# Performance work log

Hardware: AMD Instinct MI355X
Metric: run time of the kernel (lower is better)

Reference implementation:

```python
import jax, jax.numpy as jnp
import numpy as np

NUM_HEADS = 16
HEAD_SIZE = 64
LN_EPS = 1e-5


def setup_inputs() -> dict:
    key = jax.random.key(0)
    k1, k2, k3 = jax.random.split(key, 3)
    b, l, hidden = 2, 2048, 1024
    qkv_out = HEAD_SIZE * NUM_HEADS + 2 * HEAD_SIZE  # 1152
    x = jax.random.normal(k1, (b, l, hidden), dtype=jnp.float32)
    Wqkv = jax.random.normal(k2, (qkv_out, hidden), dtype=jnp.float32) * 0.02
    gamma = jnp.ones((qkv_out,), dtype=jnp.float32)
    beta = jnp.zeros((qkv_out,), dtype=jnp.float32)
    Wfc = jax.random.normal(k3, (hidden, HEAD_SIZE * NUM_HEADS), dtype=jnp.float32) * 0.02
    return {"x": x, "Wqkv": Wqkv, "gamma": gamma, "beta": beta, "Wfc": Wfc}


def reference(x, Wqkv, gamma, beta, Wfc):
    h, d = NUM_HEADS, HEAD_SIZE
    b, l, _ = x.shape
    # fused QKV projection (no bias), then LayerNorm over the FULL qkv dim
    qkv = jnp.einsum('blc,oc->blo', x, Wqkv)  # (b, l, (h+2)*d)
    mu = jnp.mean(qkv, axis=-1, keepdims=True)
    var = jnp.var(qkv, axis=-1, keepdims=True)
    qkv = (qkv - mu) * jax.lax.rsqrt(var + LN_EPS) * gamma + beta
    qkv = qkv.reshape(b, l, h + 2, d)
    k = qkv[:, :, 0, :]       # (b, l, d) shared K head
    v = qkv[:, :, 1, :]       # (b, l, d) shared V head
    q = qkv[:, :, 2:, :]      # (b, l, h, d) query heads
    scale = 1.0 / np.sqrt(d).astype(np.float32)
    scores = jnp.einsum('bqhd,bkd->bhqk', q, k) * scale  # (b, h, l, l)
    causal = jnp.tril(jnp.ones((l, l), dtype=bool))
    scores = jnp.where(causal, scores, jnp.finfo(scores.dtype).min)
    attn = jax.nn.softmax(scores, axis=-1)
    out = jnp.einsum('bhqk,bkd->bqhd', attn, v).reshape(b, l, h * d)
    return jnp.einsum('blo,ho->blh', out, Wfc)
```

## Files before the change

### kernel.cpp

```cpp
#include <hip/hip_runtime.h>
#include <stdint.h>

typedef __attribute__((ext_vector_type(8))) short s16x8;
typedef __attribute__((ext_vector_type(4))) float f32x4;

#define MFMA16(a, b, c) __builtin_amdgcn_mfma_f32_16x16x32_bf16((a), (b), (c), 0, 0, 0)

__device__ __forceinline__ unsigned short f2bf(float f) {
    unsigned int u = __float_as_uint(f);
    return (unsigned short)((u + 0x7FFFu + ((u >> 16) & 1u)) >> 16);
}
__device__ __forceinline__ float bf2f(unsigned short h) {
    return __uint_as_float(((unsigned int)h) << 16);
}
__device__ __forceinline__ void cvt8(unsigned short* dst, const float* src) {
    const float4 f0 = *(const float4*)(src);
    const float4 f1 = *(const float4*)(src + 4);
    s16x8 v;
    v[0] = (short)f2bf(f0.x); v[1] = (short)f2bf(f0.y);
    v[2] = (short)f2bf(f0.z); v[3] = (short)f2bf(f0.w);
    v[4] = (short)f2bf(f1.x); v[5] = (short)f2bf(f1.y);
    v[6] = (short)f2bf(f1.z); v[7] = (short)f2bf(f1.w);
    *(s16x8*)dst = v;
}
__device__ __forceinline__ void gl_lds16(const unsigned short* g, unsigned short* l) {
    __builtin_amdgcn_global_load_lds(
        (const __attribute__((address_space(1))) unsigned int*)g,
        (__attribute__((address_space(3))) unsigned int*)l,
        16, 0, 0);
}

__global__ __launch_bounds__(256) void cvt_all(const float* __restrict__ x,
                                               const float* __restrict__ wq,
                                               const float* __restrict__ wf,
                                               unsigned short* __restrict__ xb,
                                               unsigned short* __restrict__ wqb,
                                               unsigned short* __restrict__ wfb) {
    const int blk = blockIdx.x;
    const float* src;
    unsigned short* dst;
    int base;
    if (blk < 2048)      { src = x;  dst = xb;  base = blk; }
    else if (blk < 2624) { src = wq; dst = wqb; base = blk - 2048; }
    else                 { src = wf; dst = wfb; base = blk - 2624; }
    const int i = (base * 256 + threadIdx.x) * 8;
    cvt8(&dst[i], &src[i]);
}

template <bool OUT_F32>
__global__ __launch_bounds__(512) void gemm_mn(const unsigned short* __restrict__ A,
                                               const unsigned short* __restrict__ Bw,
                                               void* __restrict__ Cout, int K, int N) {
    const int bm = blockIdx.x, bn = blockIdx.y;
    const int t = threadIdx.x;
    const int lane = t & 63, w = t >> 6;
    const int quad = lane >> 4, col = lane & 15;
    const int wm = (w >> 1) * 32, wn = (w & 1) * 32;

    __shared__ alignas(16) unsigned short As[2][128 * 64];
    __shared__ alignas(16) unsigned short Bs[2][64 * 64];

    f32x4 acc[2][2];
#pragma unroll
    for (int i = 0; i < 2; ++i)
#pragma unroll
        for (int j = 0; j < 2; ++j) acc[i][j] = (f32x4){0.f, 0.f, 0.f, 0.f};

    const int lrow = lane >> 3;
    const int lcol = ((lane & 7) ^ lrow) * 8;
    const unsigned short* Ap = A + (size_t)(bm * 128 + w * 16 + lrow) * K + lcol;
    const unsigned short* Bp = Bw + (size_t)(bn * 64 + w * 8 + lrow) * K + lcol;

#pragma unroll
    for (int j = 0; j < 2; ++j)
        gl_lds16(Ap + (size_t)(j * 8) * K, &As[0][(w * 16 + j * 8) * 64]);
    gl_lds16(Bp, &Bs[0][(w * 8) * 64]);
    __syncthreads();

    const int c7 = col & 7;
    const int fs0 = ((0 * 4 + quad) ^ c7) * 8;
    const int fs1 = ((1 * 4 + quad) ^ c7) * 8;

    for (int k0 = 0; k0 < K; k0 += 64) {
        const int p = (k0 >> 6) & 1;
        if (k0 + 64 < K) {
#pragma unroll
            for (int j = 0; j < 2; ++j)
                gl_lds16(Ap + (size_t)(j * 8) * K + k0 + 64, &As[p ^ 1][(w * 16 + j * 8) * 64]);
            gl_lds16(Bp + k0 + 64, &Bs[p ^ 1][(w * 8) * 64]);
        }
#pragma unroll
        for (int s = 0; s < 2; ++s) {
            const int fs = s ? fs1 : fs0;
            s16x8 af[2], bfr[2];
#pragma unroll
            for (int i = 0; i < 2; ++i)
                af[i] = *(const s16x8*)&As[p][(wm + i * 16 + col) * 64 + fs];
#pragma unroll
            for (int j = 0; j < 2; ++j)
                bfr[j] = *(const s16x8*)&Bs[p][(wn + j * 16 + col) * 64 + fs];
#pragma unroll
            for (int i = 0; i < 2; ++i)
#pragma unroll
                for (int j = 0; j < 2; ++j)
                    acc[i][j] = MFMA16(af[i], bfr[j], acc[i][j]);
        }
        __syncthreads();
    }
    const int rowb = bm * 128 + wm + quad * 4;
    const int colb = bn * 64 + wn + col;
#pragma unroll
    for (int i = 0; i < 2; ++i)
#pragma unroll
        for (int j = 0; j < 2; ++j)
#pragma unroll
            for (int r = 0; r < 4; ++r) {
                size_t off = (size_t)(rowb + i * 16 + r) * N + colb + j * 16;
                if (OUT_F32) ((float*)Cout)[off] = acc[i][j][r];
                else ((unsigned short*)Cout)[off] = f2bf(acc[i][j][r]);
            }
}

__global__ __launch_bounds__(64) void ln_row(unsigned short* __restrict__ qkvn,
                                             const float* __restrict__ gamma,
                                             const float* __restrict__ beta,
                                             unsigned short* __restrict__ vT) {
    const int row = blockIdx.x;
    const int b = row >> 11, l = row & 2047;
    unsigned short* rp = qkvn + (size_t)row * 1152;
    const int lane = threadIdx.x;

    s16x8 v0 = *(const s16x8*)&rp[lane * 8];
    s16x8 v1 = *(const s16x8*)&rp[512 + lane * 8];
    unsigned int v2u = *(const unsigned int*)&rp[1024 + lane * 2];

    float f0[8], f1[8], f2[2];
    float s = 0.f, s2 = 0.f;
#pragma unroll
    for (int e = 0; e < 8; ++e) {
        f0[e] = bf2f((unsigned short)v0[e]);
        f1[e] = bf2f((unsigned short)v1[e]);
        s += f0[e] + f1[e];
        s2 += f0[e] * f0[e] + f1[e] * f1[e];
    }
    f2[0] = bf2f((unsigned short)(v2u & 0xFFFF));
    f2[1] = bf2f((unsigned short)(v2u >> 16));
    s += f2[0] + f2[1];
    s2 += f2[0] * f2[0] + f2[1] * f2[1];

#pragma unroll
    for (int off = 1; off < 64; off <<= 1) {
        s += __shfl_xor(s, off);
        s2 += __shfl_xor(s2, off);
    }
    const float mu = s * (1.0f / 1152.0f);
    float var = s2 * (1.0f / 1152.0f) - mu * mu;
    var = fmaxf(var, 0.0f);
    const float rstd = rsqrtf(var + 1e-5f);

    {
        s16x8 o;
#pragma unroll
        for (int e = 0; e < 8; ++e)
            o[e] = (short)f2bf((f0[e] - mu) * rstd * gamma[lane * 8 + e] + beta[lane * 8 + e]);
        *(s16x8*)&rp[lane * 8] = o;
        if (lane >= 8 && lane < 16) {
            const int d0 = lane * 8 - 64;
#pragma unroll
            for (int e = 0; e < 8; ++e)
                vT[((size_t)(b * 64 + d0 + e)) * 2048 + l] = (unsigned short)o[e];
        }
    }
    {
        s16x8 o;
#pragma unroll
        for (int e = 0; e < 8; ++e)
            o[e] = (short)f2bf((f1[e] - mu) * rstd * gamma[512 + lane * 8 + e] + beta[512 + lane * 8 + e]);
        *(s16x8*)&rp[512 + lane * 8] = o;
    }
    {
        unsigned short o0 = f2bf((f2[0] - mu) * rstd * gamma[1024 + lane * 2] + beta[1024 + lane * 2]);
        unsigned short o1 = f2bf((f2[1] - mu) * rstd * gamma[1025 + lane * 2] + beta[1025 + lane * 2]);
        *(unsigned int*)&rp[1024 + lane * 2] = ((unsigned int)o1 << 16) | o0;
    }
}

__global__ __launch_bounds__(512) void attn_kernel(const unsigned short* __restrict__ qkvn,
                                                   const unsigned short* __restrict__ vT,
                                                   unsigned short* __restrict__ obuf) {
    const int b = blockIdx.x >> 3, hp = blockIdx.x & 7;
    const int yy = blockIdx.y;
    const int qb = (yy < 16) ? (31 - yy) : (yy - 16);
    const int t = threadIdx.x;
    const int lane = t & 63, w = t >> 6;
    const int quad = lane >> 4, col = lane & 15;
    const int hl = w >> 2, wq = w & 3;

    __shared__ alignas(16) unsigned short Ks[2][4096];
    __shared__ alignas(16) unsigned short Vts[2][4096];
    __shared__ alignas(16) unsigned short PQ[8][16][72];

    unsigned short(*Qs)[72] = (unsigned short(*)[72])PQ;

    const int srow = t >> 3;
    const int schunk = t & 7;
    const int ldsoff = srow * 64 + (schunk ^ (srow & 7)) * 8;

#pragma unroll
    for (int hh = 0; hh < 2; ++hh) {
        const unsigned short* qsrc =
            qkvn + (size_t)(b * 2048 + qb * 64 + srow) * 1152 + 128 + (hp * 2 + hh) * 64 + schunk * 8;
        s16x8 v = *(const s16x8*)qsrc;
#pragma unroll
        for (int e = 0; e < 8; ++e)
            v[e] = (short)f2bf(bf2f((unsigned short)v[e]) * 0.125f);
        *(s16x8*)&Qs[hh * 64 + srow][schunk * 8] = v;
    }
    __syncthreads();
    const s16x8 qf0 = *(const s16x8*)&Qs[hl * 64 + wq * 16 + col][quad * 8];
    const s16x8 qf1 = *(const s16x8*)&Qs[hl * 64 + wq * 16 + col][32 + quad * 8];

    const unsigned short* kbase = qkvn + (size_t)(b * 2048 + srow) * 1152 + schunk * 8;
    const unsigned short* vbase = vT + (size_t)(b * 64 + srow) * 2048 + schunk * 8;
    *(uint4*)&Ks[0][ldsoff]  = *(const uint4*)(kbase);
    *(uint4*)&Vts[0][ldsoff] = *(const uint4*)(vbase);
    __syncthreads();

    const int fo0 = col * 128 + ((quad ^ (col & 7)) * 16);
    const int fo1 = col * 128 + (((4 + quad) ^ (col & 7)) * 16);

    s16x8 ones;
#pragma unroll
    for (int e = 0; e < 8; ++e) ones[e] = (short)0x3F80;

    f32x4 Oacc[4];
    f32x4 lacc = {0.f, 0.f, 0.f, 0.f};
#pragma unroll
    for (int nt = 0; nt < 4; ++nt) Oacc[nt] = (f32x4){0.f, 0.f, 0.f, 0.f};

    const int qglob = qb * 64 + wq * 16 + col;
    const int kloc0 = quad * 4;

    for (int kb = 0; kb <= qb; ++kb) {
        const int p = kb & 1;
        uint4 kreg, vreg;
        if (kb < qb) {
            kreg = *(const uint4*)(kbase + (size_t)(kb + 1) * 64 * 1152);
            vreg = *(const uint4*)(vbase + (kb + 1) * 64);
        }
        const bool diag = (kb == qb);
        const char* kb8 = (const char*)Ks[p];
        const char* vb8 = (const char*)Vts[p];

#pragma unroll
        for (int nt = 0; nt < 4; ++nt) {
            s16x8 kf0 = *(const s16x8*)(kb8 + nt * 2048 + fo0);
            s16x8 kf1 = *(const s16x8*)(kb8 + nt * 2048 + fo1);
            f32x4 z = (f32x4){0.f, 0.f, 0.f, 0.f};
            z = MFMA16(kf0, qf0, z);
            z = MFMA16(kf1, qf1, z);
            ushort4 pk;
            unsigned short* pp = (unsigned short*)&pk;
#pragma unroll
            for (int r = 0; r < 4; ++r) {
                float sv = z[r];
                if (diag && (kb * 64 + nt * 16 + kloc0 + r > qglob)) sv = -1e30f;
                pp[r] = f2bf(__expf(sv - 12.0f));
            }
            *(ushort4*)&PQ[w][col][nt * 16 + kloc0] = pk;
        }

        const s16x8 pf0 = *(const s16x8*)&PQ[w][col][quad * 8];
        const s16x8 pf1 = *(const s16x8*)&PQ[w][col][32 + quad * 8];
        lacc = MFMA16(ones, pf0, lacc);
        lacc = MFMA16(ones, pf1, lacc);
#pragma unroll
        for (int nt = 0; nt < 4; ++nt) {
            s16x8 vf0 = *(const s16x8*)(vb8 + nt * 2048 + fo0);
            s16x8 vf1 = *(const s16x8*)(vb8 + nt * 2048 + fo1);
            Oacc[nt] = MFMA16(vf0, pf0, Oacc[nt]);
            Oacc[nt] = MFMA16(vf1, pf1, Oacc[nt]);
        }

        if (kb < qb) {
            *(uint4*)&Ks[p ^ 1][ldsoff]  = kreg;
            *(uint4*)&Vts[p ^ 1][ldsoff] = vreg;
        }
        __syncthreads();
    }

    const int h = hp * 2 + hl;
    const float inv = 1.0f / lacc[0];
    const size_t base = (((size_t)b * 2048 + qglob) * 16 + h) * 64 + kloc0;
#pragma unroll
    for (int nt = 0; nt < 4; ++nt) {
        ushort4 ov;
        unsigned short* op = (unsigned short*)&ov;
#pragma unroll
        for (int r = 0; r < 4; ++r) op[r] = f2bf(Oacc[nt][r] * inv);
        *(ushort4*)&obuf[base + nt * 16] = ov;
    }
}

extern "C" void kernel_launch(void* const* d_in, const int* in_sizes, int n_in,
                              void* d_out, int out_size, void* d_ws, size_t ws_size,
                              hipStream_t stream) {
    (void)in_sizes; (void)n_in; (void)out_size; (void)ws_size;
    const float* x     = (const float*)d_in[0];
    const float* Wqkv  = (const float*)d_in[1];
    const float* gamma = (const float*)d_in[2];
    const float* beta  = (const float*)d_in[3];
    const float* Wfc   = (const float*)d_in[4];
    float* out = (float*)d_out;

    char* ws = (char*)d_ws;
    unsigned short* xb   = (unsigned short*)ws;
    unsigned short* Wqb  = (unsigned short*)(ws + 8388608);
    unsigned short* Wfb  = (unsigned short*)(ws + 10747904);
    unsigned short* qkvn = (unsigned short*)(ws + 12845056);
    unsigned short* vT   = (unsigned short*)(ws + 22282240);
    unsigned short* abuf = (unsigned short*)ws;

    cvt_all<<<dim3(3136), 256, 0, stream>>>(x, Wqkv, Wfc, xb, Wqb, Wfb);
    gemm_mn<false><<<dim3(32, 18), 512, 0, stream>>>(xb, Wqb, qkvn, 1024, 1152);
    ln_row<<<dim3(4096), 64, 0, stream>>>(qkvn, gamma, beta, vT);
    attn_kernel<<<dim3(16, 32), 512, 0, stream>>>(qkvn, vT, abuf);
    gemm_mn<true><<<dim3(32, 16), 512, 0, stream>>>(abuf, Wfb, out, 1024, 1024);
}
```

Baseline: 151.0 us.

## Split attention key tiles across wave pairs and reuse K/V fragments across two query tiles

Each wave now handles 32 queries and half of each 64-key block instead of 16 queries and the full block. Every K and V fragment read from LDS now feeds two query sub-tiles, which cuts LDS traffic per MFMA. Waves whose key half lies entirely above the diagonal skip work on the diagonal block. The two key halves' partial O and row sums are merged through shared memory at the end. The change also adds an occupancy hint in launch bounds and raises wave priority around the PV MFMAs, at the cost of more registers per wave and an extra reduction with a barrier.

```diff
diff --git a/kernel.cpp b/kernel.cpp
--- a/kernel.cpp
+++ b/kernel.cpp
@@ -185,22 +185,24 @@
     }
 }
 
-__global__ __launch_bounds__(512) void attn_kernel(const unsigned short* __restrict__ qkvn,
-                                                   const unsigned short* __restrict__ vT,
-                                                   unsigned short* __restrict__ obuf) {
+__global__ __launch_bounds__(512, 4) void attn_kernel(const unsigned short* __restrict__ qkvn,
+                                                      const unsigned short* __restrict__ vT,
+                                                      unsigned short* __restrict__ obuf) {
     const int b = blockIdx.x >> 3, hp = blockIdx.x & 7;
     const int yy = blockIdx.y;
     const int qb = (yy < 16) ? (31 - yy) : (yy - 16);
     const int t = threadIdx.x;
     const int lane = t & 63, w = t >> 6;
     const int quad = lane >> 4, col = lane & 15;
-    const int hl = w >> 2, wq = w & 3;
-
-    __shared__ alignas(16) unsigned short Ks[2][4096];
-    __shared__ alignas(16) unsigned short Vts[2][4096];
-    __shared__ alignas(16) unsigned short PQ[8][16][72];
-
-    unsigned short(*Qs)[72] = (unsigned short(*)[72])PQ;
+    const int hl = w >> 2;
+    const int qhalf = (w >> 1) & 1;
+    const int kpar = w & 1;
+
+    __shared__ alignas(16) unsigned char SM[53248];
+    unsigned short* Ks0 = (unsigned short*)SM;
+    unsigned short* Vt0 = (unsigned short*)(SM + 16384);
+    unsigned short* Qs  = (unsigned short*)(SM + 32768);
+    unsigned short* Ps  = (unsigned short*)(SM + 32768) + w * 1280;
 
     const int srow = t >> 3;
     const int schunk = t & 7;
@@ -214,32 +216,41 @@
 #pragma unroll
         for (int e = 0; e < 8; ++e)
             v[e] = (short)f2bf(bf2f((unsigned short)v[e]) * 0.125f);
-        *(s16x8*)&Qs[hh * 64 + srow][schunk * 8] = v;
+        *(s16x8*)&Qs[(hh * 64 + srow) * 80 + schunk * 8] = v;
     }
     __syncthreads();
-    const s16x8 qf0 = *(const s16x8*)&Qs[hl * 64 + wq * 16 + col][quad * 8];
-    const s16x8 qf1 = *(const s16x8*)&Qs[hl * 64 + wq * 16 + col][32 + quad * 8];
+    s16x8 qfr[2][2];
+#pragma unroll
+    for (int qf = 0; qf < 2; ++qf)
+#pragma unroll
+        for (int dh = 0; dh < 2; ++dh)
+            qfr[qf][dh] = *(const s16x8*)&Qs[(hl * 64 + qhalf * 32 + qf * 16 + col) * 80 + dh * 32 + quad * 8];
 
     const unsigned short* kbase = qkvn + (size_t)(b * 2048 + srow) * 1152 + schunk * 8;
     const unsigned short* vbase = vT + (size_t)(b * 64 + srow) * 2048 + schunk * 8;
-    *(uint4*)&Ks[0][ldsoff]  = *(const uint4*)(kbase);
-    *(uint4*)&Vts[0][ldsoff] = *(const uint4*)(vbase);
+    *(uint4*)&Ks0[ldsoff] = *(const uint4*)(kbase);
+    *(uint4*)&Vt0[ldsoff] = *(const uint4*)(vbase);
     __syncthreads();
 
-    const int fo0 = col * 128 + ((quad ^ (col & 7)) * 16);
-    const int fo1 = col * 128 + (((4 + quad) ^ (col & 7)) * 16);
+    const int c7 = col & 7;
+    const int koff0 = (kpar * 32 + col) * 128 + ((quad ^ c7) * 16);
+    const int koff1 = (kpar * 32 + col) * 128 + (((4 + quad) ^ c7) * 16);
+    const int voff = col * 128 + (((kpar * 4 + quad) ^ c7) * 16);
 
     s16x8 ones;
 #pragma unroll
     for (int e = 0; e < 8; ++e) ones[e] = (short)0x3F80;
 
-    f32x4 Oacc[4];
-    f32x4 lacc = {0.f, 0.f, 0.f, 0.f};
-#pragma unroll
-    for (int nt = 0; nt < 4; ++nt) Oacc[nt] = (f32x4){0.f, 0.f, 0.f, 0.f};
-
-    const int qglob = qb * 64 + wq * 16 + col;
-    const int kloc0 = quad * 4;
+    f32x4 Oacc[4][2];
+    f32x4 lacc[2];
+#pragma unroll
+    for (int ds = 0; ds < 4; ++ds)
+#pragma unroll
+        for (int qf = 0; qf < 2; ++qf) Oacc[ds][qf] = (f32x4){0.f, 0.f, 0.f, 0.f};
+    lacc[0] = (f32x4){0.f, 0.f, 0.f, 0.f};
+    lacc[1] = (f32x4){0.f, 0.f, 0.f, 0.f};
+
+    const int qbase = qb * 64 + qhalf * 32;
 
     for (int kb = 0; kb <= qb; ++kb) {
         const int p = kb & 1;
@@ -249,56 +260,85 @@
             vreg = *(const uint4*)(vbase + (kb + 1) * 64);
         }
         const bool diag = (kb == qb);
-        const char* kb8 = (const char*)Ks[p];
-        const char* vb8 = (const char*)Vts[p];
-
-#pragma unroll
-        for (int nt = 0; nt < 4; ++nt) {
-            s16x8 kf0 = *(const s16x8*)(kb8 + nt * 2048 + fo0);
-            s16x8 kf1 = *(const s16x8*)(kb8 + nt * 2048 + fo1);
-            f32x4 z = (f32x4){0.f, 0.f, 0.f, 0.f};
-            z = MFMA16(kf0, qf0, z);
-            z = MFMA16(kf1, qf1, z);
-            ushort4 pk;
-            unsigned short* pp = (unsigned short*)&pk;
-#pragma unroll
-            for (int r = 0; r < 4; ++r) {
-                float sv = z[r];
-                if (diag && (kb * 64 + nt * 16 + kloc0 + r > qglob)) sv = -1e30f;
-                pp[r] = f2bf(__expf(sv - 12.0f));
+        if (!(diag && kpar == 1 && qhalf == 0)) {
+            const bool needmask = diag && (kpar == qhalf);
+            const char* kb8 = (const char*)(Ks0 + p * 4096);
+            const char* vb8 = (const char*)(Vt0 + p * 4096);
+
+#pragma unroll
+            for (int nt = 0; nt < 2; ++nt) {
+                const s16x8 kf0 = *(const s16x8*)(kb8 + nt * 2048 + koff0);
+                const s16x8 kf1 = *(const s16x8*)(kb8 + nt * 2048 + koff1);
+#pragma unroll
+                for (int qf = 0; qf < 2; ++qf) {
+                    f32x4 z = (f32x4){0.f, 0.f, 0.f, 0.f};
+                    z = MFMA16(kf0, qfr[qf][0], z);
+                    z = MFMA16(kf1, qfr[qf][1], z);
+                    ushort4 pk;
+                    unsigned short* pp = (unsigned short*)&pk;
+                    const int qg = qbase + qf * 16 + col;
+                    const int kl = kb * 64 + kpar * 32 + nt * 16 + quad * 4;
+#pragma unroll
+                    for (int r = 0; r < 4; ++r) {
+                        float sv = z[r];
+                        if (needmask && (kl + r > qg)) sv = -1e30f;
+                        pp[r] = f2bf(__expf(sv - 12.0f));
+                    }
+                    *(ushort4*)&Ps[(qf * 16 + col) * 40 + nt * 16 + quad * 4] = pk;
+                }
             }
-            *(ushort4*)&PQ[w][col][nt * 16 + kloc0] = pk;
-        }
-
-        const s16x8 pf0 = *(const s16x8*)&PQ[w][col][quad * 8];
-        const s16x8 pf1 = *(const s16x8*)&PQ[w][col][32 + quad * 8];
-        lacc = MFMA16(ones, pf0, lacc);
-        lacc = MFMA16(ones, pf1, lacc);
-#pragma unroll
-        for (int nt = 0; nt < 4; ++nt) {
-            s16x8 vf0 = *(const s16x8*)(vb8 + nt * 2048 + fo0);
-            s16x8 vf1 = *(const s16x8*)(vb8 + nt * 2048 + fo1);
-            Oacc[nt] = MFMA16(vf0, pf0, Oacc[nt]);
-            Oacc[nt] = MFMA16(vf1, pf1, Oacc[nt]);
+
+            const s16x8 pf0 = *(const s16x8*)&Ps[col * 40 + quad * 8];
+            const s16x8 pf1 = *(const s16x8*)&Ps[(16 + col) * 40 + quad * 8];
+            __builtin_amdgcn_s_setprio(1);
+            lacc[0] = MFMA16(ones, pf0, lacc[0]);
+            lacc[1] = MFMA16(ones, pf1, lacc[1]);
+#pragma unroll
+            for (int ds = 0; ds < 4; ++ds) {
+                const s16x8 vf = *(const s16x8*)(vb8 + ds * 2048 + voff);
+                Oacc[ds][0] = MFMA16(vf, pf0, Oacc[ds][0]);
+                Oacc[ds][1] = MFMA16(vf, pf1, Oacc[ds][1]);
+            }
+            __builtin_amdgcn_s_setprio(0);
         }
 
         if (kb < qb) {
-            *(uint4*)&Ks[p ^ 1][ldsoff]  = kreg;
-            *(uint4*)&Vts[p ^ 1][ldsoff] = vreg;
+            *(uint4*)&Ks0[(p ^ 1) * 4096 + ldsoff] = kreg;
+            *(uint4*)&Vt0[(p ^ 1) * 4096 + ldsoff] = vreg;
         }
         __syncthreads();
     }
 
-    const int h = hp * 2 + hl;
-    const float inv = 1.0f / lacc[0];
-    const size_t base = (((size_t)b * 2048 + qglob) * 16 + h) * 64 + kloc0;
-#pragma unroll
-    for (int nt = 0; nt < 4; ++nt) {
-        ushort4 ov;
-        unsigned short* op = (unsigned short*)&ov;
-#pragma unroll
-        for (int r = 0; r < 4; ++r) op[r] = f2bf(Oacc[nt][r] * inv);
-        *(ushort4*)&obuf[base + nt * 16] = ov;
+    float* mg = (float*)SM + (hl * 2 + qhalf) * 2112;
+    float* lm = (float*)(SM + 33792) + (hl * 2 + qhalf) * 32;
+    if (kpar) {
+#pragma unroll
+        for (int ds = 0; ds < 4; ++ds)
+#pragma unroll
+            for (int qf = 0; qf < 2; ++qf)
+#pragma unroll
+                for (int r = 0; r < 4; ++r)
+                    mg[(ds * 16 + quad * 4 + r) * 33 + qf * 16 + col] = Oacc[ds][qf][r];
+        if (quad == 0) { lm[col] = lacc[0][0]; lm[16 + col] = lacc[1][0]; }
+    }
+    __syncthreads();
+    if (!kpar) {
+        const int h = hp * 2 + hl;
+#pragma unroll
+        for (int qf = 0; qf < 2; ++qf) {
+            const int qglob = qbase + qf * 16 + col;
+            const float inv = 1.0f / (lacc[qf][0] + lm[qf * 16 + col]);
+            const size_t base = (((size_t)b * 2048 + qglob) * 16 + h) * 64 + quad * 4;
+#pragma unroll
+            for (int ds = 0; ds < 4; ++ds) {
+                ushort4 ov;
+                unsigned short* op = (unsigned short*)&ov;
+#pragma unroll
+                for (int r = 0; r < 4; ++r)
+                    op[r] = f2bf((Oacc[ds][qf][r] + mg[(ds * 16 + quad * 4 + r) * 33 + qf * 16 + col]) * inv);
+                *(ushort4*)&obuf[base + ds * 16] = ov;
+            }
+        }
     }
 }
 
```

New measurement: 151.5 us. No clear change (+0.3%).
